# Optimization experiments

Measured on AMD Instinct MI355X. Metric: run time of the kernel, lower is better.

Reference implementation:

```python
import jax, jax.numpy as jnp
import numpy as np

D_MODEL = 1024
N_EXPERTS = 16
TOP_K = 2
EXPERT_DIM = 1024
SHARED_DIM = 2048
B, T = 2, 1024


def setup_inputs() -> dict:
    key = jax.random.key(0)
    ks = jax.random.split(key, 7)
    std = 0.02
    return {
        "x": jax.random.normal(ks[0], (B, T, D_MODEL), dtype=jnp.float32),
        "router_w": jax.random.normal(ks[1], (N_EXPERTS, D_MODEL), dtype=jnp.float32) * std,
        "gate_up_w": jax.random.normal(ks[2], (N_EXPERTS, D_MODEL, 2 * EXPERT_DIM), dtype=jnp.float32) * std,
        "down_w": jax.random.normal(ks[3], (N_EXPERTS, EXPERT_DIM, D_MODEL), dtype=jnp.float32) * std,
        "shared_gate_w": jax.random.normal(ks[4], (SHARED_DIM, D_MODEL), dtype=jnp.float32) * std,
        "shared_up_w": jax.random.normal(ks[5], (SHARED_DIM, D_MODEL), dtype=jnp.float32) * std,
        "shared_down_w": jax.random.normal(ks[6], (D_MODEL, SHARED_DIM), dtype=jnp.float32) * std,
    }


def reference(x, router_w, gate_up_w, down_w, shared_gate_w, shared_up_w, shared_down_w):
    Bb, Tt, C = x.shape
    N = Bb * Tt
    E = gate_up_w.shape[0]

    # Router: top-k logits, sigmoid gating (matches torch.topk then sigmoid).
    logits = jnp.einsum('btc,ec->bte', x, router_w)          # [B,T,E]
    top_vals, top_idx = jax.lax.top_k(logits, TOP_K)          # [B,T,K]
    gates = jax.nn.sigmoid(top_vals)

    xf = x.reshape(N, C)
    sel = top_idx.reshape(N, TOP_K)
    gw = gates.reshape(N, TOP_K)

    # Dense per-token expert gate [N,E]: zero except selected experts.
    # top_k indices are distinct per token, so scatter-add == scatter-set.
    w_full = jnp.zeros((N, E), dtype=x.dtype).at[jnp.arange(N)[:, None], sel].add(gw)

    # Run every token through every expert densely (same math as the
    # per-token gather + bmm + scatter_add combine, without materializing
    # [N*K, C, 2H] gathered weight tensors).
    gu = jnp.einsum('nc,ech->neh', xf, gate_up_w)             # [N,E,2H]
    gate, up = jnp.split(gu, 2, axis=-1)
    h = jax.nn.silu(gate) * up                                # [N,E,H]
    out_all = jnp.einsum('neh,ehc->nec', h, down_w)           # [N,E,C]
    moe = jnp.einsum('ne,nec->nc', w_full, out_all).reshape(Bb, Tt, C)

    # Shared expert (SwiGLU MLP).
    sg = jnp.einsum('btc,sc->bts', x, shared_gate_w)
    su = jnp.einsum('btc,sc->bts', x, shared_up_w)
    shared = jnp.einsum('bts,cs->btc', jax.nn.silu(sg) * su, shared_down_w)

    return moe + shared
```

## Files before the change

kernel.cpp:

```cpp
#include <hip/hip_runtime.h>
#include <cstdint>

#define N_TOK 2048
#define CDIM  1024
#define NEXP  16
#define TOPK  2
#define HDIM  1024
#define SDIM  2048
#define ESLOT 48
#define GU_EXP_BLOCKS (ESLOT * 16)
#define GU_SH_BLOCKS  (16 * 32)
#define GU_NWG (GU_EXP_BLOCKS + GU_SH_BLOCKS)
#define DW_CONV_BLOCKS 2048
#define GU9X_NWG (GU_NWG + DW_CONV_BLOCKS)
#define DN_EXP_BLOCKS (ESLOT * 8)
#define DN_SH_BLOCKS  (16 * 8)
#define DN_NWG (DN_EXP_BLOCKS + DN_SH_BLOCKS)
#define PREP_GUW_TILES 8192
#define PREP_NWG (1 + PREP_GUW_TILES + 3072)

typedef __bf16 bf16;
typedef __bf16 bf16x8 __attribute__((ext_vector_type(8)));
typedef float  f32x4  __attribute__((ext_vector_type(4)));
typedef unsigned int u32;
typedef unsigned short u16;

typedef __attribute__((address_space(3))) uint32_t lds_u32_t;
typedef __attribute__((address_space(1))) uint32_t glb_u32_t;

__device__ __forceinline__ void gload16(const void* g, void* l) {
  __builtin_amdgcn_global_load_lds((const glb_u32_t*)(uintptr_t)g,
                                   (lds_u32_t*)(uintptr_t)l, 16, 0, 0);
}
__device__ __forceinline__ float fromb(u16 s) {
  union { float f; u32 u; } z; z.u = ((u32)s) << 16; return z.f;
}
__device__ __forceinline__ int xcd_swz(int bid, int nwg) {
  return (bid & 7) * (nwg >> 3) + (bid >> 3);
}
#define SBAR0() __builtin_amdgcn_sched_barrier(0)
#define WAIT_VM(N) do { asm volatile("s_waitcnt vmcnt(" #N ")" ::: "memory"); \
                        SBAR0(); } while (0)

__device__ __forceinline__ void conv_tile(const float* __restrict__ s,
                                          bf16* __restrict__ d,
                                          int K, int N, int k0, int n0,
                                          int t, float* ld) {
  const int kk = t >> 4, c4 = (t & 15) * 4;
#pragma unroll
  for (int q = 0; q < 4; ++q) {
    float4 f = *(const float4*)(s + (size_t)(k0 + kk + q * 16) * N + n0 + c4);
    float* lp = &ld[(kk + q * 16) * 68 + c4];
    lp[0] = f.x; lp[1] = f.y; lp[2] = f.z; lp[3] = f.w;
  }
  __syncthreads();
  const int nn = t >> 2, kc = (t & 3) * 16;
  bf16x8 v0, v1;
#pragma unroll
  for (int j = 0; j < 8; ++j) {
    v0[j] = (bf16)ld[(kc + j) * 68 + nn];
    v1[j] = (bf16)ld[(kc + 8 + j) * 68 + nn];
  }
  bf16* dp = d + (size_t)(n0 + nn) * K + k0 + kc;
  *(bf16x8*)dp = v0;
  *(bf16x8*)(dp + 8) = v1;
}

__global__ __launch_bounds__(256)
void router_kernel(const float* __restrict__ x,
                   const float* __restrict__ rw,
                   bf16* __restrict__ xb,
                   int* __restrict__ sel,
                   float* __restrict__ gatew) {
  int n = blockIdx.x * 4 + (threadIdx.x >> 6);
  int lane = threadIdx.x & 63;
  const float* xr = x + (size_t)n * CDIM;
  float xv[16];
#pragma unroll
  for (int q = 0; q < 4; ++q) {
    float4 f = *(const float4*)(xr + lane * 16 + q * 4);
    xv[q * 4 + 0] = f.x; xv[q * 4 + 1] = f.y; xv[q * 4 + 2] = f.z; xv[q * 4 + 3] = f.w;
  }
  bf16x8 v0, v1;
#pragma unroll
  for (int j = 0; j < 8; ++j) { v0[j] = (bf16)xv[j]; v1[j] = (bf16)xv[8 + j]; }
  bf16* xo = xb + (size_t)n * CDIM + lane * 16;
  *(bf16x8*)xo = v0;
  *(bf16x8*)(xo + 8) = v1;
  float acc[NEXP];
#pragma unroll
  for (int e = 0; e < NEXP; ++e) {
    float a = 0.f;
    const float* rwe = rw + e * CDIM + lane * 16;
#pragma unroll
    for (int j = 0; j < 16; ++j) a += xv[j] * rwe[j];
    acc[e] = a;
  }
#pragma unroll
  for (int off = 32; off > 0; off >>= 1) {
#pragma unroll
    for (int e = 0; e < NEXP; ++e) acc[e] += __shfl_xor(acc[e], off, 64);
  }
  if (lane == 0) {
    int i0 = 0; float v0_ = acc[0];
#pragma unroll
    for (int e = 1; e < NEXP; ++e) if (acc[e] > v0_) { v0_ = acc[e]; i0 = e; }
    int i1 = (i0 == 0) ? 1 : 0; float v1_ = acc[i1];
#pragma unroll
    for (int e = 0; e < NEXP; ++e) if (e != i0 && acc[e] > v1_) { v1_ = acc[e]; i1 = e; }
    sel[2 * n] = i0; sel[2 * n + 1] = i1;
    gatew[2 * n]     = 1.f / (1.f + expf(-v0_));
    gatew[2 * n + 1] = 1.f / (1.f + expf(-v1_));
  }
}

__global__ __launch_bounds__(256)
void prep_kernel(const float* __restrict__ guw,
                 const float* __restrict__ sgw,
                 const float* __restrict__ suw,
                 const float* __restrict__ sdw,
                 bf16* __restrict__ guw_b,
                 bf16* __restrict__ sgw_b,
                 bf16* __restrict__ suw_b,
                 bf16* __restrict__ sdw_b,
                 const int* __restrict__ sel,
                 const float* __restrict__ gatew,
                 int* __restrict__ counts,
                 int* __restrict__ offsets,
                 int* __restrict__ tab128,
                 int* __restrict__ ntiles,
                 int* __restrict__ entry_token,
                 float* __restrict__ entry_gate,
                 int* __restrict__ entry_pos) {
  __shared__ __align__(16) float ld[64 * 68];
  const int b = blockIdx.x;
  const int t = threadIdx.x;
  if (b == 0) {
    int* hist = (int*)ld;
    int* cur = hist + NEXP;
    if (t < NEXP) hist[t] = 0;
    __syncthreads();
    for (int i = t; i < N_TOK * TOPK; i += 256) atomicAdd(&hist[sel[i]], 1);
    __syncthreads();
    if (t == 0) {
      int s = 0, a = 0;
      for (int e = 0; e < NEXP; ++e) {
        int c = hist[e];
        counts[e] = c; offsets[e] = s; cur[e] = s;
        for (int m0 = 0; m0 < c; m0 += 128) tab128[a++] = (e << 16) | m0;
        s += c;
      }
      ntiles[0] = a;
    }
    __syncthreads();
    for (int i = t; i < N_TOK * TOPK; i += 256) {
      int e = sel[i];
      int pos = atomicAdd(&cur[e], 1);
      entry_token[pos] = i >> 1;
      entry_gate[pos] = gatew[i];
      entry_pos[i] = pos;
    }
    return;
  }
  if (b <= PREP_GUW_TILES) {
    const int idx = b - 1;
    const int e = idx >> 9;
    const int rem = idx & 511;
    const int n0 = (rem & 31) << 6;
    const int k0 = (rem >> 5) << 6;
    conv_tile(guw + (size_t)e * CDIM * 2 * HDIM,
              guw_b + (size_t)e * 2 * HDIM * CDIM,
              CDIM, 2 * HDIM, k0, n0, t, ld);
    return;
  }
  const int b2 = b - 1 - PREP_GUW_TILES;
  const float* s; bf16* d;
  if (b2 < 1024)      { s = sgw; d = sgw_b; }
  else if (b2 < 2048) { s = suw; d = suw_b; }
  else                { s = sdw; d = sdw_b; }
  int i = ((b2 & 1023) * 256 + t) * 8;
  float4 f0 = *(const float4*)(s + i);
  float4 f1 = *(const float4*)(s + i + 4);
  bf16x8 v;
  v[0]=(bf16)f0.x; v[1]=(bf16)f0.y; v[2]=(bf16)f0.z; v[3]=(bf16)f0.w;
  v[4]=(bf16)f1.x; v[5]=(bf16)f1.y; v[6]=(bf16)f1.z; v[7]=(bf16)f1.w;
  *(bf16x8*)(d + i) = v;
}

__global__ __launch_bounds__(512, 2)
void gu9x(const bf16* __restrict__ xb,
          const bf16* __restrict__ guwb,
          const bf16* __restrict__ sgwb,
          const bf16* __restrict__ suwb,
          bf16* __restrict__ h_exp,
          bf16* __restrict__ h_sh,
          const int* __restrict__ counts,
          const int* __restrict__ offsets,
          const int* __restrict__ entry_token,
          const int* __restrict__ tab128,
          const int* __restrict__ ntiles,
          const float* __restrict__ dw,
          bf16* __restrict__ dw_b) {
  __shared__ __align__(16) char smem[81920];
  bf16* sA  = (bf16*)smem;
  bf16* sBg = (bf16*)(smem + 32768);
  bf16* sBu = (bf16*)(smem + 57344);

  const int t = threadIdx.x;

  if (blockIdx.x >= GU_NWG) {
    const int tid2 = (blockIdx.x - GU_NWG) * 2 + (t >> 8);
    float* ld = (float*)(smem + (t >> 8) * 17408);
    const int e = tid2 >> 8;
    const int rem = tid2 & 255;
    const int n0c = (rem & 15) << 6;
    const int k0c = (rem >> 4) << 6;
    conv_tile(dw + (size_t)e * HDIM * CDIM,
              dw_b + (size_t)e * CDIM * HDIM,
              HDIM, CDIM, k0c, n0c, t & 255, ld);
    return;
  }

  const int bid = xcd_swz(blockIdx.x, GU_NWG);
  const bool is_exp = bid < GU_EXP_BLOCKS;
  const int wid = t >> 6, lane = t & 63;

  int n0, mguard;
  bf16* hbase; int hstride;
  const bf16 *Bg, *Bu;
  const int arow = t >> 3;
  const int sc = (t & 7) ^ (arow & 7);
  const bf16* asrc[2];

  if (is_exp) {
    const int slot = bid >> 4;
    if (slot >= ntiles[0]) return;
    const int packed = tab128[slot];
    const int e = packed >> 16;
    const int m0 = packed & 0xffff;
    const int cnt = counts[e];
    const int base = offsets[e];
    n0 = (bid & 15) * 64;
    mguard = cnt - m0;
#pragma unroll
    for (int i = 0; i < 2; ++i) {
      int r = m0 + i * 64 + arow;
      int tok = entry_token[base + ((r < cnt) ? r : (cnt - 1))];
      asrc[i] = xb + (size_t)tok * CDIM + sc * 8;
    }
    const bf16* we = guwb + (size_t)e * (2 * HDIM) * CDIM;
    Bg = we + (size_t)n0 * CDIM;
    Bu = we + (size_t)(HDIM + n0) * CDIM;
    hbase = h_exp + (size_t)(base + m0) * HDIM + n0;
    hstride = HDIM;
  } else {
    const int sid = bid - GU_EXP_BLOCKS;
    const int m0 = (sid >> 5) * 128;
    n0 = (sid & 31) * 64;
    mguard = 128;
#pragma unroll
    for (int i = 0; i < 2; ++i)
      asrc[i] = xb + (size_t)(m0 + i * 64 + arow) * CDIM + sc * 8;
    Bg = sgwb + (size_t)n0 * CDIM;
    Bu = suwb + (size_t)n0 * CDIM;
    hbase = h_sh + (size_t)m0 * SDIM + n0;
    hstride = SDIM;
  }

  const int th = t & 255;
  bf16* bdst = (t >= 256) ? sBu : sBg;
  const bf16* Bp = (t >= 256) ? Bu : Bg;
  const bf16* bsrc[2];
#pragma unroll
  for (int i = 0; i < 2; ++i) {
    const int row = i * 32 + (th >> 3);
    const int c = (th & 7) ^ (row & 7);
    bsrc[i] = Bp + (size_t)row * CDIM + c * 8;
  }
  const int adst = t * 8;
  const int bdoff = th * 8;

#define ISSUE_A(k_, ab_)                                                      \
  do {                                                                        \
    _Pragma("unroll")                                                         \
    for (int i = 0; i < 2; ++i)                                               \
      gload16(asrc[i] + (k_), &sA[(ab_) * 8192 + i * 4096 + adst]);           \
  } while (0)
#define ISSUE_B(k_, bo_)                                                      \
  do {                                                                        \
    _Pragma("unroll")                                                         \
    for (int i = 0; i < 2; ++i)                                               \
      gload16(bsrc[i] + (k_), &bdst[(bo_) + i * 2048 + bdoff]);               \
  } while (0)

  const int wr = (wid >> 1) * 32, wc = (wid & 1) * 32;
  const int lrow = lane & 15, grp = lane >> 4;

  f32x4 ag[2][2], au[2][2];
#pragma unroll
  for (int m = 0; m < 2; ++m)
#pragma unroll
    for (int n = 0; n < 2; ++n)
#pragma unroll
      for (int i = 0; i < 4; ++i) { ag[m][n][i] = 0.f; au[m][n][i] = 0.f; }

#define COMPUTE(ab_, bo_)                                                     \
  do {                                                                        \
    _Pragma("unroll")                                                         \
    for (int ks = 0; ks < 2; ++ks) {                                          \
      const int ch = ks * 4 + grp;                                            \
      bf16x8 av[2], bg[2], bu[2];                                             \
      _Pragma("unroll")                                                       \
      for (int m = 0; m < 2; ++m) {                                           \
        const int r = wr + m * 16 + lrow;                                     \
        av[m] = *(const bf16x8*)&sA[(ab_) * 8192 + r * 64 + ((ch ^ (r & 7)) << 3)]; \
      }                                                                       \
      _Pragma("unroll")                                                       \
      for (int n = 0; n < 2; ++n) {                                           \
        const int r = wc + n * 16 + lrow;                                     \
        const int so = r * 64 + ((ch ^ (r & 7)) << 3);                        \
        bg[n] = *(const bf16x8*)&sBg[(bo_) + so];                             \
        bu[n] = *(const bf16x8*)&sBu[(bo_) + so];                             \
      }                                                                       \
      _Pragma("unroll")                                                       \
      for (int m = 0; m < 2; ++m)                                             \
        _Pragma("unroll")                                                     \
        for (int n = 0; n < 2; ++n) {                                         \
          ag[m][n] = __builtin_amdgcn_mfma_f32_16x16x32_bf16(av[m], bg[n], ag[m][n], 0, 0, 0); \
          au[m][n] = __builtin_amdgcn_mfma_f32_16x16x32_bf16(av[m], bu[n], au[m][n], 0, 0, 0); \
        }                                                                     \
    }                                                                         \
  } while (0)

  ISSUE_A(0, 0);
  ISSUE_B(0, 0);
  SBAR0();
  ISSUE_B(64, 4096);
  SBAR0();
  WAIT_VM(2);
  __builtin_amdgcn_s_barrier();

  int bb0 = 0, bb1 = 4096, bb2 = 8192;
  for (int k = 0; k < 14; ++k) {
    ISSUE_A((k + 1) * 64, (k + 1) & 1);
    SBAR0();
    ISSUE_B((k + 2) * 64, bb2);
    SBAR0();
    COMPUTE(k & 1, bb0);
    WAIT_VM(2);
    __builtin_amdgcn_s_barrier();
    int tmp = bb0; bb0 = bb1; bb1 = bb2; bb2 = tmp;
  }
  ISSUE_A(15 * 64, 1);
  SBAR0();
  COMPUTE(0, bb0);
  WAIT_VM(0);
  __builtin_amdgcn_s_barrier();
  { int tmp = bb0; bb0 = bb1; bb1 = bb2; bb2 = tmp; }
  COMPUTE(1, bb0);
#undef ISSUE_A
#undef ISSUE_B
#undef COMPUTE

#pragma unroll
  for (int m = 0; m < 2; ++m) {
#pragma unroll
    for (int i = 0; i < 4; ++i) {
      const int rl = wr + m * 16 + grp * 4 + i;
      if (rl >= mguard) continue;
      bf16* orow = hbase + (size_t)rl * hstride;
#pragma unroll
      for (int n = 0; n < 2; ++n) {
        const float g = ag[m][n][i];
        const float u = au[m][n][i];
        orow[wc + n * 16 + lrow] = (bf16)(g * u * __builtin_amdgcn_rcpf(1.f + __expf(-g)));
      }
    }
  }
}

__global__ __launch_bounds__(512, 2)
void dn9(const bf16* __restrict__ h_exp,
         const bf16* __restrict__ h_sh,
         const bf16* __restrict__ dwb,
         const bf16* __restrict__ sdwb,
         const float* __restrict__ entry_gate,
         bf16* __restrict__ out_e,
         float* __restrict__ out,
         const int* __restrict__ counts,
         const int* __restrict__ offsets,
         const int* __restrict__ tab128,
         const int* __restrict__ ntiles) {
  __shared__ __align__(16) bf16 sA[2 * 8192];
  __shared__ __align__(16) bf16 sB[3 * 8192];

  const int bid = xcd_swz(blockIdx.x, DN_NWG);
  const int t = threadIdx.x;
  const bool is_exp = bid < DN_EXP_BLOCKS;
  const int wid = t >> 6, lane = t & 63;

  int n0, mguard, K, rowbase, NK;
  const bf16* Ab;
  const bf16* Bb;

  if (is_exp) {
    const int slot = bid >> 3;
    if (slot >= ntiles[0]) return;
    const int packed = tab128[slot];
    const int e = packed >> 16;
    const int m0 = packed & 0xffff;
    const int cnt = counts[e];
    n0 = (bid & 7) * 128;
    mguard = cnt - m0;
    K = HDIM; NK = HDIM / 64;
    rowbase = offsets[e] + m0;
    Ab = h_exp;
    Bb = dwb + (size_t)e * CDIM * HDIM + (size_t)n0 * HDIM;
  } else {
    const int sid = bid - DN_EXP_BLOCKS;
    const int m0 = (sid >> 3) * 128;
    n0 = (sid & 7) * 128;
    mguard = 128;
    K = SDIM; NK = SDIM / 64;
    rowbase = m0;
    Ab = h_sh;
    Bb = sdwb + (size_t)n0 * SDIM;
  }

  const int arow = t >> 3;
  const int sc = (t & 7) ^ (arow & 7);
  const bf16* asrc[2];
#pragma unroll
  for (int i = 0; i < 2; ++i) {
    int rg = rowbase + i * 64 + arow;
    if (is_exp && rg > N_TOK * TOPK - 1) rg = N_TOK * TOPK - 1;
    asrc[i] = Ab + (size_t)rg * K + sc * 8;
  }
  const bf16* bsrc[2];
#pragma unroll
  for (int i = 0; i < 2; ++i)
    bsrc[i] = Bb + (size_t)(i * 64 + arow) * K + sc * 8;
  const int adst = t * 8;

#define ISSUE_A(k_, ab_)                                                      \
  do {                                                                        \
    _Pragma("unroll")                                                         \
    for (int i = 0; i < 2; ++i)                                               \
      gload16(asrc[i] + (k_), &sA[(ab_) * 8192 + i * 4096 + adst]);           \
  } while (0)
#define ISSUE_B(k_, bo_)                                                      \
  do {                                                                        \
    _Pragma("unroll")                                                         \
    for (int i = 0; i < 2; ++i)                                               \
      gload16(bsrc[i] + (k_), &sB[(bo_) + i * 4096 + adst]);                  \
  } while (0)

  const int wr = (wid >> 1) * 32, wc = (wid & 1) * 64;
  const int lrow = lane & 15, grp = lane >> 4;

  f32x4 acc[2][4];
#pragma unroll
  for (int m = 0; m < 2; ++m)
#pragma unroll
    for (int n = 0; n < 4; ++n)
#pragma unroll
      for (int i = 0; i < 4; ++i) acc[m][n][i] = 0.f;

#define COMPUTE(ab_, bo_)                                                     \
  do {                                                                        \
    _Pragma("unroll")                                                         \
    for (int ks = 0; ks < 2; ++ks) {                                          \
      const int ch = ks * 4 + grp;                                            \
      bf16x8 av[2], bv[4];                                                    \
      _Pragma("unroll")                                                       \
      for (int m = 0; m < 2; ++m) {                                           \
        const int r = wr + m * 16 + lrow;                                     \
        av[m] = *(const bf16x8*)&sA[(ab_) * 8192 + r * 64 + ((ch ^ (r & 7)) << 3)]; \
      }                                                                       \
      _Pragma("unroll")                                                       \
      for (int n = 0; n < 4; ++n) {                                           \
        const int r = wc + n * 16 + lrow;                                     \
        bv[n] = *(const bf16x8*)&sB[(bo_) + r * 64 + ((ch ^ (r & 7)) << 3)];  \
      }                                                                       \
      _Pragma("unroll")                                                       \
      for (int m = 0; m < 2; ++m)                                             \
        _Pragma("unroll")                                                     \
        for (int n = 0; n < 4; ++n)                                           \
          acc[m][n] = __builtin_amdgcn_mfma_f32_16x16x32_bf16(av[m], bv[n], acc[m][n], 0, 0, 0); \
    }                                                                         \
  } while (0)

  ISSUE_A(0, 0);
  ISSUE_B(0, 0);
  SBAR0();
  ISSUE_B(64, 8192);
  SBAR0();
  WAIT_VM(2);
  __builtin_amdgcn_s_barrier();

  int bb0 = 0, bb1 = 8192, bb2 = 16384;
  for (int k = 0; k < NK - 2; ++k) {
    ISSUE_A((k + 1) * 64, (k + 1) & 1);
    SBAR0();
    ISSUE_B((k + 2) * 64, bb2);
    SBAR0();
    COMPUTE(k & 1, bb0);
    WAIT_VM(2);
    __builtin_amdgcn_s_barrier();
    int tmp = bb0; bb0 = bb1; bb1 = bb2; bb2 = tmp;
  }
  ISSUE_A((NK - 1) * 64, (NK - 1) & 1);
  SBAR0();
  COMPUTE((NK - 2) & 1, bb0);
  WAIT_VM(0);
  __builtin_amdgcn_s_barrier();
  { int tmp = bb0; bb0 = bb1; bb1 = bb2; bb2 = tmp; }
  COMPUTE((NK - 1) & 1, bb0);
#undef ISSUE_A
#undef ISSUE_B
#undef COMPUTE

#pragma unroll
  for (int m = 0; m < 2; ++m) {
#pragma unroll
    for (int i = 0; i < 4; ++i) {
      const int rl = wr + m * 16 + grp * 4 + i;
      if (rl >= mguard) continue;
      if (is_exp) {
        const int row = rowbase + rl;
        const float scl = entry_gate[row];
        bf16* orow = out_e + (size_t)row * CDIM + n0;
#pragma unroll
        for (int n = 0; n < 4; ++n)
          orow[wc + n * 16 + lrow] = (bf16)(acc[m][n][i] * scl);
      } else {
        float* orow = out + (size_t)(rowbase + rl) * CDIM + n0;
#pragma unroll
        for (int n = 0; n < 4; ++n)
          orow[wc + n * 16 + lrow] = acc[m][n][i];
      }
    }
  }
}

__global__ void combine_kernel(float* __restrict__ out,
                               const bf16* __restrict__ out_e,
                               const int* __restrict__ entry_pos) {
  int tid = blockIdx.x * blockDim.x + threadIdx.x;
  int n = tid >> 8;
  int c4 = tid & 255;
  int p0 = entry_pos[2 * n];
  int p1 = entry_pos[2 * n + 1];
  float4 v = ((const float4*)out)[tid];
  ushort4 a = *(const ushort4*)((const u16*)out_e + (size_t)p0 * CDIM + c4 * 4);
  ushort4 b = *(const ushort4*)((const u16*)out_e + (size_t)p1 * CDIM + c4 * 4);
  v.x += fromb(a.x) + fromb(b.x);
  v.y += fromb(a.y) + fromb(b.y);
  v.z += fromb(a.z) + fromb(b.z);
  v.w += fromb(a.w) + fromb(b.w);
  ((float4*)out)[tid] = v;
}

extern "C" void kernel_launch(void* const* d_in, const int* in_sizes, int n_in,
                              void* d_out, int out_size, void* d_ws, size_t ws_size,
                              hipStream_t stream) {
  const float* x   = (const float*)d_in[0];
  const float* rw  = (const float*)d_in[1];
  const float* guw = (const float*)d_in[2];
  const float* dw  = (const float*)d_in[3];
  const float* sgw = (const float*)d_in[4];
  const float* suw = (const float*)d_in[5];
  const float* sdw = (const float*)d_in[6];
  float* out = (float*)d_out;
  char* ws = (char*)d_ws;
  const size_t MB = 1048576;

  int*   sel         = (int*)(ws + 0);
  float* gatew       = (float*)(ws + 16384);
  int*   counts      = (int*)(ws + 32768);
  int*   offsets     = (int*)(ws + 32832);
  int*   ntiles      = (int*)(ws + 32960);
  int*   tab128      = (int*)(ws + 33024);
  int*   entry_token = (int*)(ws + 33664);
  float* entry_gate  = (float*)(ws + 50048);
  int*   entry_pos   = (int*)(ws + 66432);

  bf16* xb    = (bf16*)(ws + 82816);
  bf16* h_exp = (bf16*)(ws + 82816 + 4 * MB);
  bf16* h_sh  = (bf16*)(ws + 82816 + 12 * MB);
  bf16* sgw_b = (bf16*)(ws + 82816 + 20 * MB);
  bf16* suw_b = (bf16*)(ws + 82816 + 24 * MB);
  bf16* guw_b = (bf16*)(ws + 82816 + 28 * MB);
  bf16* dw_b  = (bf16*)(ws + 82816 + 92 * MB);
  bf16* sdw_b = (bf16*)(ws + 82816 + 124 * MB);
  bf16* out_e = sgw_b;

  router_kernel<<<N_TOK / 4, 256, 0, stream>>>(x, rw, xb, sel, gatew);

  prep_kernel<<<PREP_NWG, 256, 0, stream>>>(guw, sgw, suw, sdw,
                                            guw_b, sgw_b, suw_b, sdw_b,
                                            sel, gatew, counts, offsets, tab128,
                                            ntiles, entry_token, entry_gate, entry_pos);

  gu9x<<<GU9X_NWG, 512, 0, stream>>>(xb, guw_b, sgw_b, suw_b, h_exp, h_sh,
                                     counts, offsets, entry_token, tab128, ntiles,
                                     dw, dw_b);

  dn9<<<DN_NWG, 512, 0, stream>>>(h_exp, h_sh, dw_b, sdw_b, entry_gate, out_e, out,
                                  counts, offsets, tab128, ntiles);

  combine_kernel<<<(N_TOK * CDIM / 4) / 256, 256, 0, stream>>>(out, out_e, entry_pos);
}
```

Measured before the change: 158.9 us.

## Keep expert weights in K-major layout and read B fragments with LDS transpose loads

The gate/up and down expert weights are now converted to bf16 in their original [K,N] layout with a plain elementwise cast, instead of a transposing tile conversion through LDS. The GEMM kernels then stage B tiles in a packed 16-column layout and build MFMA B operands with ds_read_b64_tr_b16 transpose reads. A operands are read with paired ds_read_b64 loads. The shared-expert weights go the other way and are now transposed in the prep kernel. This removes the LDS round trip and strided stores for the large expert weight conversion. The costs are more LDS read instructions and an explicit lgkmcnt(0) wait in every compute step, which may hurt overlap.

```diff
diff --git a/kernel.cpp b/kernel.cpp
--- a/kernel.cpp
+++ b/kernel.cpp
@@ -11,22 +11,26 @@
 #define GU_EXP_BLOCKS (ESLOT * 16)
 #define GU_SH_BLOCKS  (16 * 32)
 #define GU_NWG (GU_EXP_BLOCKS + GU_SH_BLOCKS)
-#define DW_CONV_BLOCKS 2048
+#define DW_CONV_BLOCKS 4096
 #define GU9X_NWG (GU_NWG + DW_CONV_BLOCKS)
 #define DN_EXP_BLOCKS (ESLOT * 8)
 #define DN_SH_BLOCKS  (16 * 8)
 #define DN_NWG (DN_EXP_BLOCKS + DN_SH_BLOCKS)
-#define PREP_GUW_TILES 8192
-#define PREP_NWG (1 + PREP_GUW_TILES + 3072)
+#define PREP_GUW_BLKS 16384
+#define PREP_SH_BLKS  1536
+#define PREP_NWG (1 + PREP_GUW_BLKS + PREP_SH_BLKS)
 
 typedef __bf16 bf16;
 typedef __bf16 bf16x8 __attribute__((ext_vector_type(8)));
 typedef float  f32x4  __attribute__((ext_vector_type(4)));
 typedef unsigned int u32;
+typedef u32 u32x2 __attribute__((ext_vector_type(2)));
 typedef unsigned short u16;
 
 typedef __attribute__((address_space(3))) uint32_t lds_u32_t;
 typedef __attribute__((address_space(1))) uint32_t glb_u32_t;
+
+union FragU { u32 w[4]; bf16x8 v; };
 
 __device__ __forceinline__ void gload16(const void* g, void* l) {
   __builtin_amdgcn_global_load_lds((const glb_u32_t*)(uintptr_t)g,
@@ -41,6 +45,8 @@
 #define SBAR0() __builtin_amdgcn_sched_barrier(0)
 #define WAIT_VM(N) do { asm volatile("s_waitcnt vmcnt(" #N ")" ::: "memory"); \
                         SBAR0(); } while (0)
+#define WAIT_LGKM0() do { asm volatile("s_waitcnt lgkmcnt(0)" ::: "memory"); \
+                          SBAR0(); } while (0)
 
 __device__ __forceinline__ void conv_tile(const float* __restrict__ s,
                                           bf16* __restrict__ d,
@@ -119,10 +125,10 @@
                  const float* __restrict__ sgw,
                  const float* __restrict__ suw,
                  const float* __restrict__ sdw,
-                 bf16* __restrict__ guw_b,
-                 bf16* __restrict__ sgw_b,
-                 bf16* __restrict__ suw_b,
-                 bf16* __restrict__ sdw_b,
+                 bf16* __restrict__ guw_bk,
+                 bf16* __restrict__ sgw_bk,
+                 bf16* __restrict__ suw_bk,
+                 bf16* __restrict__ sdw_bk,
                  const int* __restrict__ sel,
                  const float* __restrict__ gatew,
                  int* __restrict__ counts,
@@ -162,36 +168,33 @@
     }
     return;
   }
-  if (b <= PREP_GUW_TILES) {
-    const int idx = b - 1;
-    const int e = idx >> 9;
-    const int rem = idx & 511;
-    const int n0 = (rem & 31) << 6;
-    const int k0 = (rem >> 5) << 6;
-    conv_tile(guw + (size_t)e * CDIM * 2 * HDIM,
-              guw_b + (size_t)e * 2 * HDIM * CDIM,
-              CDIM, 2 * HDIM, k0, n0, t, ld);
+  if (b <= PREP_GUW_BLKS) {
+    size_t i = (size_t)(b - 1) * 2048 + t * 8;
+    float4 f0 = *(const float4*)(guw + i);
+    float4 f1 = *(const float4*)(guw + i + 4);
+    bf16x8 v;
+    v[0]=(bf16)f0.x; v[1]=(bf16)f0.y; v[2]=(bf16)f0.z; v[3]=(bf16)f0.w;
+    v[4]=(bf16)f1.x; v[5]=(bf16)f1.y; v[6]=(bf16)f1.z; v[7]=(bf16)f1.w;
+    *(bf16x8*)(guw_bk + i) = v;
     return;
   }
-  const int b2 = b - 1 - PREP_GUW_TILES;
-  const float* s; bf16* d;
-  if (b2 < 1024)      { s = sgw; d = sgw_b; }
-  else if (b2 < 2048) { s = suw; d = suw_b; }
-  else                { s = sdw; d = sdw_b; }
-  int i = ((b2 & 1023) * 256 + t) * 8;
-  float4 f0 = *(const float4*)(s + i);
-  float4 f1 = *(const float4*)(s + i + 4);
-  bf16x8 v;
-  v[0]=(bf16)f0.x; v[1]=(bf16)f0.y; v[2]=(bf16)f0.z; v[3]=(bf16)f0.w;
-  v[4]=(bf16)f1.x; v[5]=(bf16)f1.y; v[6]=(bf16)f1.z; v[7]=(bf16)f1.w;
-  *(bf16x8*)(d + i) = v;
+  const int b2 = b - 1 - PREP_GUW_BLKS;
+  const int which = b2 >> 9;
+  const int tile = b2 & 511;
+  if (which == 0) {
+    conv_tile(sgw, sgw_bk, SDIM, CDIM, (tile >> 4) * 64, (tile & 15) * 64, t, ld);
+  } else if (which == 1) {
+    conv_tile(suw, suw_bk, SDIM, CDIM, (tile >> 4) * 64, (tile & 15) * 64, t, ld);
+  } else {
+    conv_tile(sdw, sdw_bk, CDIM, SDIM, (tile >> 5) * 64, (tile & 31) * 64, t, ld);
+  }
 }
 
 __global__ __launch_bounds__(512, 2)
-void gu9x(const bf16* __restrict__ xb,
-          const bf16* __restrict__ guwb,
-          const bf16* __restrict__ sgwb,
-          const bf16* __restrict__ suwb,
+void gu10(const bf16* __restrict__ xb,
+          const bf16* __restrict__ guw_bk,
+          const bf16* __restrict__ sgw_bk,
+          const bf16* __restrict__ suw_bk,
           bf16* __restrict__ h_exp,
           bf16* __restrict__ h_sh,
           const int* __restrict__ counts,
@@ -200,24 +203,21 @@
           const int* __restrict__ tab128,
           const int* __restrict__ ntiles,
           const float* __restrict__ dw,
-          bf16* __restrict__ dw_b) {
-  __shared__ __align__(16) char smem[81920];
-  bf16* sA  = (bf16*)smem;
-  bf16* sBg = (bf16*)(smem + 32768);
-  bf16* sBu = (bf16*)(smem + 57344);
+          bf16* __restrict__ dw_bk) {
+  __shared__ __align__(16) bf16 sA[2 * 8192];
+  __shared__ __align__(16) bf16 sBg[3 * 4096];
+  __shared__ __align__(16) bf16 sBu[3 * 4096];
 
   const int t = threadIdx.x;
 
   if (blockIdx.x >= GU_NWG) {
-    const int tid2 = (blockIdx.x - GU_NWG) * 2 + (t >> 8);
-    float* ld = (float*)(smem + (t >> 8) * 17408);
-    const int e = tid2 >> 8;
-    const int rem = tid2 & 255;
-    const int n0c = (rem & 15) << 6;
-    const int k0c = (rem >> 4) << 6;
-    conv_tile(dw + (size_t)e * HDIM * CDIM,
-              dw_b + (size_t)e * CDIM * HDIM,
-              HDIM, CDIM, k0c, n0c, t & 255, ld);
+    size_t i = (size_t)(blockIdx.x - GU_NWG) * 4096 + t * 8;
+    float4 f0 = *(const float4*)(dw + i);
+    float4 f1 = *(const float4*)(dw + i + 4);
+    bf16x8 v;
+    v[0]=(bf16)f0.x; v[1]=(bf16)f0.y; v[2]=(bf16)f0.z; v[3]=(bf16)f0.w;
+    v[4]=(bf16)f1.x; v[5]=(bf16)f1.y; v[6]=(bf16)f1.z; v[7]=(bf16)f1.w;
+    *(bf16x8*)(dw_bk + i) = v;
     return;
   }
 
@@ -227,7 +227,7 @@
 
   int n0, mguard;
   bf16* hbase; int hstride;
-  const bf16 *Bg, *Bu;
+  const bf16 *gbase, *ubase;
   const int arow = t >> 3;
   const int sc = (t & 7) ^ (arow & 7);
   const bf16* asrc[2];
@@ -248,9 +248,9 @@
       int tok = entry_token[base + ((r < cnt) ? r : (cnt - 1))];
       asrc[i] = xb + (size_t)tok * CDIM + sc * 8;
     }
-    const bf16* we = guwb + (size_t)e * (2 * HDIM) * CDIM;
-    Bg = we + (size_t)n0 * CDIM;
-    Bu = we + (size_t)(HDIM + n0) * CDIM;
+    const bf16* we = guw_bk + (size_t)e * CDIM * (2 * HDIM);
+    gbase = we + n0;
+    ubase = we + HDIM + n0;
     hbase = h_exp + (size_t)(base + m0) * HDIM + n0;
     hstride = HDIM;
   } else {
@@ -261,21 +261,24 @@
 #pragma unroll
     for (int i = 0; i < 2; ++i)
       asrc[i] = xb + (size_t)(m0 + i * 64 + arow) * CDIM + sc * 8;
-    Bg = sgwb + (size_t)n0 * CDIM;
-    Bu = suwb + (size_t)n0 * CDIM;
+    gbase = sgw_bk + n0;
+    ubase = suw_bk + n0;
     hbase = h_sh + (size_t)m0 * SDIM + n0;
     hstride = SDIM;
   }
 
   const int th = t & 255;
   bf16* bdst = (t >= 256) ? sBu : sBg;
-  const bf16* Bp = (t >= 256) ? Bu : Bg;
+  const bf16* Bp = (t >= 256) ? ubase : gbase;
   const bf16* bsrc[2];
 #pragma unroll
   for (int i = 0; i < 2; ++i) {
-    const int row = i * 32 + (th >> 3);
-    const int c = (th & 7) ^ (row & 7);
-    bsrc[i] = Bp + (size_t)row * CDIM + c * 8;
+    const int el2 = th * 8 + i * 2048;
+    const int np = el2 >> 10;
+    const int rem = el2 & 1023;
+    const int kk = rem >> 4;
+    const int n8 = (rem >> 3) & 1;
+    bsrc[i] = Bp + (size_t)kk * (2 * HDIM) + np * 16 + n8 * 8;
   }
   const int adst = t * 8;
   const int bdoff = th * 8;
@@ -290,7 +293,8 @@
   do {                                                                        \
     _Pragma("unroll")                                                         \
     for (int i = 0; i < 2; ++i)                                               \
-      gload16(bsrc[i] + (k_), &bdst[(bo_) + i * 2048 + bdoff]);               \
+      gload16(bsrc[i] + (size_t)(k_) * (2 * HDIM),                            \
+              &bdst[(bo_) + i * 2048 + bdoff]);                               \
   } while (0)
 
   const int wr = (wid >> 1) * 32, wc = (wid & 1) * 32;
@@ -308,26 +312,50 @@
   do {                                                                        \
     _Pragma("unroll")                                                         \
     for (int ks = 0; ks < 2; ++ks) {                                          \
-      const int ch = ks * 4 + grp;                                            \
-      bf16x8 av[2], bg[2], bu[2];                                             \
+      u32x2 ra[2][2], rg[2][2], ru[2][2];                                     \
       _Pragma("unroll")                                                       \
       for (int m = 0; m < 2; ++m) {                                           \
         const int r = wr + m * 16 + lrow;                                     \
-        av[m] = *(const bf16x8*)&sA[(ab_) * 8192 + r * 64 + ((ch ^ (r & 7)) << 3)]; \
+        _Pragma("unroll")                                                     \
+        for (int h = 0; h < 2; ++h) {                                         \
+          const int c = ks * 4 + h * 2 + (grp >> 1);                          \
+          const u32 aaddr = (u32)(uintptr_t)&sA[(ab_) * 8192 + r * 64 +       \
+                              ((c ^ (r & 7)) << 3) + (grp & 1) * 4];          \
+          asm volatile("ds_read_b64 %0, %1" : "=v"(ra[m][h]) : "v"(aaddr));   \
+        }                                                                     \
       }                                                                       \
       _Pragma("unroll")                                                       \
       for (int n = 0; n < 2; ++n) {                                           \
-        const int r = wc + n * 16 + lrow;                                     \
-        const int so = r * 64 + ((ch ^ (r & 7)) << 3);                        \
-        bg[n] = *(const bf16x8*)&sBg[(bo_) + so];                             \
-        bu[n] = *(const bf16x8*)&sBu[(bo_) + so];                             \
+        const int np = (wid & 1) * 2 + n;                                     \
+        _Pragma("unroll")                                                     \
+        for (int h = 0; h < 2; ++h) {                                         \
+          const int eb = (bo_) + np * 1024 + (ks * 32 + h * 16) * 16;         \
+          const u32 ga = (u32)(uintptr_t)&sBg[eb] + lane * 8;                 \
+          const u32 ua = (u32)(uintptr_t)&sBu[eb] + lane * 8;                 \
+          asm volatile("ds_read_b64_tr_b16 %0, %1" : "=v"(rg[n][h]) : "v"(ga)); \
+          asm volatile("ds_read_b64_tr_b16 %0, %1" : "=v"(ru[n][h]) : "v"(ua)); \
+        }                                                                     \
+      }                                                                       \
+      WAIT_LGKM0();                                                           \
+      FragU fa[2], fg[2], fu[2];                                              \
+      _Pragma("unroll")                                                       \
+      for (int m = 0; m < 2; ++m) {                                           \
+        fa[m].w[0] = ra[m][0][0]; fa[m].w[1] = ra[m][0][1];                   \
+        fa[m].w[2] = ra[m][1][0]; fa[m].w[3] = ra[m][1][1];                   \
+      }                                                                       \
+      _Pragma("unroll")                                                       \
+      for (int n = 0; n < 2; ++n) {                                           \
+        fg[n].w[0] = rg[n][0][0]; fg[n].w[1] = rg[n][0][1];                   \
+        fg[n].w[2] = rg[n][1][0]; fg[n].w[3] = rg[n][1][1];                   \
+        fu[n].w[0] = ru[n][0][0]; fu[n].w[1] = ru[n][0][1];                   \
+        fu[n].w[2] = ru[n][1][0]; fu[n].w[3] = ru[n][1][1];                   \
       }                                                                       \
       _Pragma("unroll")                                                       \
       for (int m = 0; m < 2; ++m)                                             \
         _Pragma("unroll")                                                     \
         for (int n = 0; n < 2; ++n) {                                         \
-          ag[m][n] = __builtin_amdgcn_mfma_f32_16x16x32_bf16(av[m], bg[n], ag[m][n], 0, 0, 0); \
-          au[m][n] = __builtin_amdgcn_mfma_f32_16x16x32_bf16(av[m], bu[n], au[m][n], 0, 0, 0); \
+          ag[m][n] = __builtin_amdgcn_mfma_f32_16x16x32_bf16(fa[m].v, fg[n].v, ag[m][n], 0, 0, 0); \
+          au[m][n] = __builtin_amdgcn_mfma_f32_16x16x32_bf16(fa[m].v, fu[n].v, au[m][n], 0, 0, 0); \
         }                                                                     \
     }                                                                         \
   } while (0)
@@ -380,17 +408,17 @@
 }
 
 __global__ __launch_bounds__(512, 2)
-void dn9(const bf16* __restrict__ h_exp,
-         const bf16* __restrict__ h_sh,
-         const bf16* __restrict__ dwb,
-         const bf16* __restrict__ sdwb,
-         const float* __restrict__ entry_gate,
-         bf16* __restrict__ out_e,
-         float* __restrict__ out,
-         const int* __restrict__ counts,
-         const int* __restrict__ offsets,
-         const int* __restrict__ tab128,
-         const int* __restrict__ ntiles) {
+void dn10(const bf16* __restrict__ h_exp,
+          const bf16* __restrict__ h_sh,
+          const bf16* __restrict__ dw_bk,
+          const bf16* __restrict__ sdw_bk,
+          const float* __restrict__ entry_gate,
+          bf16* __restrict__ out_e,
+          float* __restrict__ out,
+          const int* __restrict__ counts,
+          const int* __restrict__ offsets,
+          const int* __restrict__ tab128,
+          const int* __restrict__ ntiles) {
   __shared__ __align__(16) bf16 sA[2 * 8192];
   __shared__ __align__(16) bf16 sB[3 * 8192];
 
@@ -415,7 +443,7 @@
     K = HDIM; NK = HDIM / 64;
     rowbase = offsets[e] + m0;
     Ab = h_exp;
-    Bb = dwb + (size_t)e * CDIM * HDIM + (size_t)n0 * HDIM;
+    Bb = dw_bk + (size_t)e * HDIM * CDIM + n0;
   } else {
     const int sid = bid - DN_EXP_BLOCKS;
     const int m0 = (sid >> 3) * 128;
@@ -424,7 +452,7 @@
     K = SDIM; NK = SDIM / 64;
     rowbase = m0;
     Ab = h_sh;
-    Bb = sdwb + (size_t)n0 * SDIM;
+    Bb = sdw_bk + n0;
   }
 
   const int arow = t >> 3;
@@ -438,8 +466,14 @@
   }
   const bf16* bsrc[2];
 #pragma unroll
-  for (int i = 0; i < 2; ++i)
-    bsrc[i] = Bb + (size_t)(i * 64 + arow) * K + sc * 8;
+  for (int i = 0; i < 2; ++i) {
+    const int el2 = t * 8 + i * 4096;
+    const int np = el2 >> 10;
+    const int rem = el2 & 1023;
+    const int kk = rem >> 4;
+    const int n8 = (rem >> 3) & 1;
+    bsrc[i] = Bb + (size_t)kk * CDIM + np * 16 + n8 * 8;
+  }
   const int adst = t * 8;
 
 #define ISSUE_A(k_, ab_)                                                      \
@@ -452,7 +486,8 @@
   do {                                                                        \
     _Pragma("unroll")                                                         \
     for (int i = 0; i < 2; ++i)                                               \
-      gload16(bsrc[i] + (k_), &sB[(bo_) + i * 4096 + adst]);                  \
+      gload16(bsrc[i] + (size_t)(k_) * CDIM,                                  \
+              &sB[(bo_) + i * 4096 + adst]);                                  \
   } while (0)
 
   const int wr = (wid >> 1) * 32, wc = (wid & 1) * 64;
@@ -470,23 +505,45 @@
   do {                                                                        \
     _Pragma("unroll")                                                         \
     for (int ks = 0; ks < 2; ++ks) {                                          \
-      const int ch = ks * 4 + grp;                                            \
-      bf16x8 av[2], bv[4];                                                    \
+      u32x2 ra[2][2], rb[4][2];                                               \
       _Pragma("unroll")                                                       \
       for (int m = 0; m < 2; ++m) {                                           \
         const int r = wr + m * 16 + lrow;                                     \
-        av[m] = *(const bf16x8*)&sA[(ab_) * 8192 + r * 64 + ((ch ^ (r & 7)) << 3)]; \
+        _Pragma("unroll")                                                     \
+        for (int h = 0; h < 2; ++h) {                                         \
+          const int c = ks * 4 + h * 2 + (grp >> 1);                          \
+          const u32 aaddr = (u32)(uintptr_t)&sA[(ab_) * 8192 + r * 64 +       \
+                              ((c ^ (r & 7)) << 3) + (grp & 1) * 4];          \
+          asm volatile("ds_read_b64 %0, %1" : "=v"(ra[m][h]) : "v"(aaddr));   \
+        }                                                                     \
       }                                                                       \
       _Pragma("unroll")                                                       \
       for (int n = 0; n < 4; ++n) {                                           \
-        const int r = wc + n * 16 + lrow;                                     \
-        bv[n] = *(const bf16x8*)&sB[(bo_) + r * 64 + ((ch ^ (r & 7)) << 3)];  \
+        const int np = (wid & 1) * 4 + n;                                     \
+        _Pragma("unroll")                                                     \
+        for (int h = 0; h < 2; ++h) {                                         \
+          const int eb = (bo_) + np * 1024 + (ks * 32 + h * 16) * 16;         \
+          const u32 ba = (u32)(uintptr_t)&sB[eb] + lane * 8;                  \
+          asm volatile("ds_read_b64_tr_b16 %0, %1" : "=v"(rb[n][h]) : "v"(ba)); \
+        }                                                                     \
+      }                                                                       \
+      WAIT_LGKM0();                                                           \
+      FragU fa[2], fb[4];                                                     \
+      _Pragma("unroll")                                                       \
+      for (int m = 0; m < 2; ++m) {                                           \
+        fa[m].w[0] = ra[m][0][0]; fa[m].w[1] = ra[m][0][1];                   \
+        fa[m].w[2] = ra[m][1][0]; fa[m].w[3] = ra[m][1][1];                   \
+      }                                                                       \
+      _Pragma("unroll")                                                       \
+      for (int n = 0; n < 4; ++n) {                                           \
+        fb[n].w[0] = rb[n][0][0]; fb[n].w[1] = rb[n][0][1];                   \
+        fb[n].w[2] = rb[n][1][0]; fb[n].w[3] = rb[n][1][1];                   \
       }                                                                       \
       _Pragma("unroll")                                                       \
       for (int m = 0; m < 2; ++m)                                             \
         _Pragma("unroll")                                                     \
         for (int n = 0; n < 4; ++n)                                           \
-          acc[m][n] = __builtin_amdgcn_mfma_f32_16x16x32_bf16(av[m], bv[n], acc[m][n], 0, 0, 0); \
+          acc[m][n] = __builtin_amdgcn_mfma_f32_16x16x32_bf16(fa[m].v, fb[n].v, acc[m][n], 0, 0, 0); \
     }                                                                         \
   } while (0)
 
@@ -585,29 +642,29 @@
   float* entry_gate  = (float*)(ws + 50048);
   int*   entry_pos   = (int*)(ws + 66432);
 
-  bf16* xb    = (bf16*)(ws + 82816);
-  bf16* h_exp = (bf16*)(ws + 82816 + 4 * MB);
-  bf16* h_sh  = (bf16*)(ws + 82816 + 12 * MB);
-  bf16* sgw_b = (bf16*)(ws + 82816 + 20 * MB);
-  bf16* suw_b = (bf16*)(ws + 82816 + 24 * MB);
-  bf16* guw_b = (bf16*)(ws + 82816 + 28 * MB);
-  bf16* dw_b  = (bf16*)(ws + 82816 + 92 * MB);
-  bf16* sdw_b = (bf16*)(ws + 82816 + 124 * MB);
-  bf16* out_e = sgw_b;
+  bf16* xb     = (bf16*)(ws + 82816);
+  bf16* h_exp  = (bf16*)(ws + 82816 + 4 * MB);
+  bf16* h_sh   = (bf16*)(ws + 82816 + 12 * MB);
+  bf16* sgw_bk = (bf16*)(ws + 82816 + 20 * MB);
+  bf16* suw_bk = (bf16*)(ws + 82816 + 24 * MB);
+  bf16* guw_bk = (bf16*)(ws + 82816 + 28 * MB);
+  bf16* dw_bk  = (bf16*)(ws + 82816 + 92 * MB);
+  bf16* sdw_bk = (bf16*)(ws + 82816 + 124 * MB);
+  bf16* out_e  = sgw_bk;
 
   router_kernel<<<N_TOK / 4, 256, 0, stream>>>(x, rw, xb, sel, gatew);
 
   prep_kernel<<<PREP_NWG, 256, 0, stream>>>(guw, sgw, suw, sdw,
-                                            guw_b, sgw_b, suw_b, sdw_b,
+                                            guw_bk, sgw_bk, suw_bk, sdw_bk,
                                             sel, gatew, counts, offsets, tab128,
                                             ntiles, entry_token, entry_gate, entry_pos);
 
-  gu9x<<<GU9X_NWG, 512, 0, stream>>>(xb, guw_b, sgw_b, suw_b, h_exp, h_sh,
+  gu10<<<GU9X_NWG, 512, 0, stream>>>(xb, guw_bk, sgw_bk, suw_bk, h_exp, h_sh,
                                      counts, offsets, entry_token, tab128, ntiles,
-                                     dw, dw_b);
-
-  dn9<<<DN_NWG, 512, 0, stream>>>(h_exp, h_sh, dw_b, sdw_b, entry_gate, out_e, out,
-                                  counts, offsets, tab128, ntiles);
+                                     dw, dw_bk);
+
+  dn10<<<DN_NWG, 512, 0, stream>>>(h_exp, h_sh, dw_bk, sdw_bk, entry_gate, out_e, out,
+                                   counts, offsets, tab128, ntiles);
 
   combine_kernel<<<(N_TOK * CDIM / 4) / 256, 256, 0, stream>>>(out, out_e, entry_pos);
 }
```

Result: slower. 170.3 us, median of 2 (+7.2%).
